# Kernel optimization log

Measured on AMD Instinct MI355X. Metric: run time of the kernel, lower is better.

## Reference

```python
import jax, jax.numpy as jnp
import numpy as np

B, S, D, C = 8, 4096, 512, 2048


def setup_inputs() -> dict:
    key = jax.random.key(0)
    kx, kc = jax.random.split(key)
    x = jax.random.normal(kx, (B, S, D), dtype=jnp.float32)
    # kaiming_uniform_(a=sqrt(5)) on a [*,D,C] tensor ~ U(-bound, bound); exact init
    # distribution is irrelevant for the math, so plain scaled uniform is used.
    bound = 1.0 / np.sqrt(D)
    codebook = jax.random.uniform(kc, (1, 1, D, C), dtype=jnp.float32,
                                  minval=-bound, maxval=bound)
    return {"x": x, "codebook": codebook}


def reference(x, codebook):
    # Original: ((x[..., :, None] - codebook) ** 2).mean(dim=-2) -> [B, S, C]
    # Equivalent GEMM form: mean_d(x_d^2) + mean_d(c_dk^2) - (2/D) * x . c_k
    d = x.shape[-1]
    cb = codebook.reshape(codebook.shape[-2], codebook.shape[-1])  # [D, C]
    x2 = jnp.mean(x * x, axis=-1, keepdims=True)                   # [B, S, 1]
    c2 = jnp.mean(cb * cb, axis=0)                                 # [C]
    xc = jnp.einsum('bsd,dc->bsc', x, cb) / d                      # [B, S, C]
    return x2 + c2 - 2.0 * xc
```

## Files before the change

### kernel.cpp

```cpp
#include <hip/hip_runtime.h>
#include <hip/hip_bf16.h>


typedef __attribute__((ext_vector_type(8))) short bf16x8;
typedef __attribute__((ext_vector_type(4))) float f32x4;

#define M_ROWS 32768
#define K_DIM  512
#define N_COLS 2048

__device__ __forceinline__ unsigned short f2bf(float f) {
    unsigned int u = __float_as_uint(f);
    return (unsigned short)((u + 0x7fffu + ((u >> 16) & 1u)) >> 16);
}

__device__ __forceinline__ void gload_lds16(const void* g, void* l) {
    __builtin_amdgcn_global_load_lds(
        (const __attribute__((address_space(1))) unsigned int*)g,
        (__attribute__((address_space(3))) unsigned int*)l,
        16, 0, 0);
}

__global__ __launch_bounds__(256) void prep_x_kernel(const float* __restrict__ x,
                                                     unsigned short* __restrict__ xb,
                                                     float* __restrict__ x2) {
    const int wid = threadIdx.x >> 6;
    const int lane = threadIdx.x & 63;
    const int row = (blockIdx.x << 2) + wid;
    const float4* p4 = reinterpret_cast<const float4*>(x + (size_t)row * K_DIM);
    float4 v0 = p4[lane];
    float4 v1 = p4[lane + 64];
    float ss = v0.x*v0.x + v0.y*v0.y + v0.z*v0.z + v0.w*v0.w
             + v1.x*v1.x + v1.y*v1.y + v1.z*v1.z + v1.w*v1.w;
    union { unsigned short us[4]; uint2 u2; } pa, pb;
    pa.us[0] = f2bf(v0.x); pa.us[1] = f2bf(v0.y); pa.us[2] = f2bf(v0.z); pa.us[3] = f2bf(v0.w);
    pb.us[0] = f2bf(v1.x); pb.us[1] = f2bf(v1.y); pb.us[2] = f2bf(v1.z); pb.us[3] = f2bf(v1.w);
    uint2* dst = reinterpret_cast<uint2*>(xb + (size_t)row * K_DIM);
    dst[lane]      = pa.u2;
    dst[lane + 64] = pb.u2;
    #pragma unroll
    for (int off = 32; off; off >>= 1) ss += __shfl_xor(ss, off);
    if (lane == 0) x2[row] = ss * (1.0f / (float)K_DIM);
}

__global__ __launch_bounds__(256) void prep_cb_kernel(const float* __restrict__ cb,
                                                      unsigned short* __restrict__ cbT) {
    __shared__ float tile[32][65];
    const int k0 = blockIdx.x * 32;
    const int n0 = blockIdx.y * 64;
    const int tx = threadIdx.x & 63;
    const int ty = threadIdx.x >> 6;
    #pragma unroll
    for (int i = 0; i < 8; ++i) {
        const int k = ty + i * 4;
        tile[k][tx] = cb[(size_t)(k0 + k) * N_COLS + n0 + tx];
    }
    __syncthreads();
    const int kc = threadIdx.x & 31;
    const int nr = threadIdx.x >> 5;
    #pragma unroll
    for (int i = 0; i < 8; ++i) {
        const int n = nr + i * 8;
        cbT[(size_t)(n0 + n) * K_DIM + k0 + kc] = f2bf(tile[kc][n] * 0.00390625f);
    }
}

__global__ __launch_bounds__(256) void c2_kernel(const float* __restrict__ cb,
                                                 float* __restrict__ c2) {
    __shared__ float p[4][64];
    const int t = threadIdx.x;
    const int nl = t & 63;
    const int kc = t >> 6;
    const int n = blockIdx.x * 64 + nl;
    float s = 0.0f;
    for (int k = kc * 128; k < kc * 128 + 128; ++k) {
        float v = cb[(size_t)k * N_COLS + n];
        s += v * v;
    }
    p[kc][nl] = s;
    __syncthreads();
    if (t < 64) {
        c2[blockIdx.x * 64 + t] =
            (p[0][t] + p[1][t] + p[2][t] + p[3][t]) * (1.0f / (float)K_DIM);
    }
}


__device__ __forceinline__ bf16x8 frag_ld(const unsigned short* h, int r, int lhi) {
    const int off = r * 32 + ((lhi ^ ((r >> 1) & 3)) << 3);
    return *reinterpret_cast<const bf16x8*>(&h[off]);
}

#define BAR()  do { asm volatile("" ::: "memory"); \
                    __builtin_amdgcn_s_barrier();  \
                    asm volatile("" ::: "memory"); } while (0)
#define GATE_(n) asm volatile("s_waitcnt vmcnt(" #n ")" ::: "memory")
#define GATE(n) GATE_(n)

__global__ __launch_bounds__(256, 2) void gemm_kernel(
        const unsigned short* __restrict__ A,
        const unsigned short* __restrict__ Bt,
        const float* __restrict__ x2,
        const float* __restrict__ c2,
        float* __restrict__ out) {
    __shared__ unsigned short smem[3][8192];

    const int tid  = threadIdx.x;
    const int wid  = tid >> 6;
    const int lane = tid & 63;
    const int wr64 = (wid >> 1) * 64;
    const int wc64 = (wid & 1) * 64;
    const int l15 = lane & 15;
    const int lhi = lane >> 4;

    const int bid  = blockIdx.x;
    const int lbid = (bid & 7) * 512 + (bid >> 3);
    const int m0 = (lbid >> 4) * 128;
    const int n0 = (lbid & 15) * 128;

    const unsigned short* Ab = A  + (size_t)m0 * K_DIM;
    const unsigned short* Bb = Bt + (size_t)n0 * K_DIM;

    const int c0   = tid;
    const int row0 = c0 >> 2;
    const size_t off0 = (size_t)row0 * K_DIM + ((size_t)(((c0 & 3) ^ ((row0 >> 1) & 3)) * 8));
    const int c1   = 256 + tid;
    const int row1 = c1 >> 2;
    const size_t off1 = (size_t)row1 * K_DIM + ((size_t)(((c1 & 3) ^ ((row1 >> 1) & 3)) * 8));

    f32x4 acc[4][4] = {};

#define STAGE(KT, BUF) do {                                                    \
    gload_lds16(Ab + off0 + (KT) * 32, &smem[(BUF)][wid * 512]);               \
    gload_lds16(Ab + off1 + (KT) * 32, &smem[(BUF)][2048 + wid * 512]);        \
    gload_lds16(Bb + off0 + (KT) * 32, &smem[(BUF)][4096 + wid * 512]);        \
    gload_lds16(Bb + off1 + (KT) * 32, &smem[(BUF)][6144 + wid * 512]); } while (0)

    STAGE(0, 0);
    STAGE(1, 1);
    GATE(4);
    BAR();

    #pragma unroll
    for (int t = 0; t < 16; ++t) {
        if (t < 14) STAGE(t + 2, (t + 2) % 3);
        const unsigned short* cbuf = smem[t % 3];
        bf16x8 b[4];
        #pragma unroll
        for (int nf = 0; nf < 4; ++nf)
            b[nf] = frag_ld(cbuf + 4096, wc64 + nf * 16 + l15, lhi);
        __builtin_amdgcn_s_setprio(1);
        #pragma unroll
        for (int mf = 0; mf < 4; ++mf) {
            const bf16x8 a = frag_ld(cbuf, wr64 + mf * 16 + l15, lhi);
            #pragma unroll
            for (int nf = 0; nf < 4; ++nf)
                acc[mf][nf] = __builtin_amdgcn_mfma_f32_16x16x32_bf16(a, b[nf], acc[mf][nf], 0, 0, 0);
        }
        __builtin_amdgcn_s_setprio(0);
        if (t < 14) { GATE(4); } else if (t == 14) { GATE(0); }
        BAR();
    }
#undef STAGE

    #pragma unroll
    for (int mf = 0; mf < 4; ++mf) {
        const int mrow = m0 + wr64 + mf * 16 + lhi * 4;
        const float xv0 = x2[mrow + 0];
        const float xv1 = x2[mrow + 1];
        const float xv2 = x2[mrow + 2];
        const float xv3 = x2[mrow + 3];
        #pragma unroll
        for (int nf = 0; nf < 4; ++nf) {
            const int col = n0 + wc64 + nf * 16 + l15;
            const float cv = c2[col];
            float* o = out + (size_t)mrow * N_COLS + col;
            o[0 * N_COLS] = xv0 + cv - acc[mf][nf][0];
            o[1 * N_COLS] = xv1 + cv - acc[mf][nf][1];
            o[2 * N_COLS] = xv2 + cv - acc[mf][nf][2];
            o[3 * N_COLS] = xv3 + cv - acc[mf][nf][3];
        }
    }
}

extern "C" void kernel_launch(void* const* d_in, const int* in_sizes, int n_in,
                              void* d_out, int out_size, void* d_ws, size_t ws_size,
                              hipStream_t stream) {
    const float* x  = (const float*)d_in[0];
    const float* cb = (const float*)d_in[1];
    float* out = (float*)d_out;

    char* ws = (char*)d_ws;
    unsigned short* xb  = (unsigned short*)ws;
    unsigned short* cbT = (unsigned short*)(ws + (size_t)33554432);
    float* x2 = (float*)(ws + (size_t)33554432 + 2097152);
    float* c2 = (float*)(ws + (size_t)33554432 + 2097152 + 131072);

    prep_x_kernel<<<M_ROWS / 4, 256, 0, stream>>>(x, xb, x2);
    prep_cb_kernel<<<dim3(16, 32), 256, 0, stream>>>(cb, cbT);
    c2_kernel<<<N_COLS / 64, 256, 0, stream>>>(cb, c2);
    gemm_kernel<<<dim3((M_ROWS / 128) * (N_COLS / 128)), 256, 0, stream>>>(xb, cbT, x2, c2, out);
}
```

Before: 126.9 us.

## Process two N-tiles per block and overlap first tile's stores with second GEMM

Each block now computes two adjacent 128-column output tiles sequentially, running one continuous 32-step K pipeline. The epilogue stores for the first tile are interleaved into the second tile's main loop, so output writes overlap MFMA work instead of sitting in a serial tail. The goal is to hide the large fp32 output write cost. In exchange each block holds two accumulator sets, which raises register pressure and may lower occupancy, and the A tile is reloaded for the second pass.

```diff
diff --git a/kernel.cpp b/kernel.cpp
--- a/kernel.cpp
+++ b/kernel.cpp
@@ -114,12 +114,14 @@
     const int lhi = lane >> 4;
 
     const int bid  = blockIdx.x;
-    const int lbid = (bid & 7) * 512 + (bid >> 3);
-    const int m0 = (lbid >> 4) * 128;
-    const int n0 = (lbid & 15) * 128;
-
-    const unsigned short* Ab = A  + (size_t)m0 * K_DIM;
-    const unsigned short* Bb = Bt + (size_t)n0 * K_DIM;
+    const int lbid = (bid & 7) * 256 + (bid >> 3);
+    const int m0  = (lbid >> 3) * 128;
+    const int n0A = (lbid & 7) * 256;
+    const int n0B = n0A + 128;
+
+    const unsigned short* Ab  = A  + (size_t)m0 * K_DIM;
+    const unsigned short* BbA = Bt + (size_t)n0A * K_DIM;
+    const unsigned short* BbB = Bt + (size_t)n0B * K_DIM;
 
     const int c0   = tid;
     const int row0 = c0 >> 2;
@@ -128,59 +130,91 @@
     const int row1 = c1 >> 2;
     const size_t off1 = (size_t)row1 * K_DIM + ((size_t)(((c1 & 3) ^ ((row1 >> 1) & 3)) * 8));
 
-    f32x4 acc[4][4] = {};
-
-#define STAGE(KT, BUF) do {                                                    \
-    gload_lds16(Ab + off0 + (KT) * 32, &smem[(BUF)][wid * 512]);               \
-    gload_lds16(Ab + off1 + (KT) * 32, &smem[(BUF)][2048 + wid * 512]);        \
-    gload_lds16(Bb + off0 + (KT) * 32, &smem[(BUF)][4096 + wid * 512]);        \
-    gload_lds16(Bb + off1 + (KT) * 32, &smem[(BUF)][6144 + wid * 512]); } while (0)
-
-    STAGE(0, 0);
-    STAGE(1, 1);
+    f32x4 accA[4][4] = {};
+    f32x4 accB[4][4] = {};
+
+    float x2v[16];
+    #pragma unroll
+    for (int mf = 0; mf < 4; ++mf)
+        #pragma unroll
+        for (int jj = 0; jj < 4; ++jj)
+            x2v[mf * 4 + jj] = x2[m0 + wr64 + mf * 16 + lhi * 4 + jj];
+    float c2oA[4];
+    #pragma unroll
+    for (int nf = 0; nf < 4; ++nf) c2oA[nf] = c2[n0A + wc64 + nf * 16 + l15];
+    float* const outA = out + (size_t)(m0 + wr64 + lhi * 4) * N_COLS + n0A + wc64 + l15;
+
+#define STAGE(KT) do {                                                         \
+    const unsigned short* bb_ = ((KT) < 16) ? BbA : BbB;                       \
+    const size_t ko_ = (size_t)(((KT) & 15) * 32);                             \
+    gload_lds16(Ab  + off0 + ko_, &smem[(KT) % 3][wid * 512]);                 \
+    gload_lds16(Ab  + off1 + ko_, &smem[(KT) % 3][2048 + wid * 512]);          \
+    gload_lds16(bb_ + off0 + ko_, &smem[(KT) % 3][4096 + wid * 512]);          \
+    gload_lds16(bb_ + off1 + ko_, &smem[(KT) % 3][6144 + wid * 512]); } while (0)
+
+#define STORE1(IDX) do {                                                       \
+    const int i_ = (IDX);                                                      \
+    const int mf_ = i_ >> 4, nf_ = (i_ >> 2) & 3, jj_ = i_ & 3;                \
+    outA[(size_t)(mf_ * 16 + jj_) * N_COLS + nf_ * 16] =                       \
+        x2v[mf_ * 4 + jj_] + c2oA[nf_] - accA[mf_][nf_][jj_]; } while (0)
+
+#define STEP(S, ACC, GN, DOG, DOST)                                            \
+  {                                                                            \
+    if ((S) <= 29) STAGE((S) + 2);                                             \
+    const unsigned short* cbuf = smem[(S) % 3];                                \
+    bf16x8 b[4];                                                               \
+    _Pragma("unroll")                                                          \
+    for (int nf = 0; nf < 4; ++nf)                                             \
+        b[nf] = frag_ld(cbuf + 4096, wc64 + nf * 16 + l15, lhi);               \
+    __builtin_amdgcn_s_setprio(1);                                             \
+    _Pragma("unroll")                                                          \
+    for (int mf = 0; mf < 4; ++mf) {                                           \
+        const bf16x8 a = frag_ld(cbuf, wr64 + mf * 16 + l15, lhi);             \
+        _Pragma("unroll")                                                      \
+        for (int nf = 0; nf < 4; ++nf)                                         \
+            ACC[mf][nf] = __builtin_amdgcn_mfma_f32_16x16x32_bf16(a, b[nf], ACC[mf][nf], 0, 0, 0); \
+    }                                                                          \
+    __builtin_amdgcn_s_setprio(0);                                             \
+    if (DOG) { GATE(GN); }                                                     \
+    if (DOST) { STORE1(((S) - 16) * 4 + 0); STORE1(((S) - 16) * 4 + 1);        \
+                STORE1(((S) - 16) * 4 + 2); STORE1(((S) - 16) * 4 + 3); }      \
+    BAR();                                                                     \
+  }
+
+    STAGE(0);
+    STAGE(1);
     GATE(4);
     BAR();
 
-    #pragma unroll
-    for (int t = 0; t < 16; ++t) {
-        if (t < 14) STAGE(t + 2, (t + 2) % 3);
-        const unsigned short* cbuf = smem[t % 3];
-        bf16x8 b[4];
+    STEP(0,  accA, 4, 1, 0) STEP(1,  accA, 4, 1, 0) STEP(2,  accA, 4, 1, 0)
+    STEP(3,  accA, 4, 1, 0) STEP(4,  accA, 4, 1, 0) STEP(5,  accA, 4, 1, 0)
+    STEP(6,  accA, 4, 1, 0) STEP(7,  accA, 4, 1, 0) STEP(8,  accA, 4, 1, 0)
+    STEP(9,  accA, 4, 1, 0) STEP(10, accA, 4, 1, 0) STEP(11, accA, 4, 1, 0)
+    STEP(12, accA, 4, 1, 0) STEP(13, accA, 4, 1, 0) STEP(14, accA, 4, 1, 0)
+    STEP(15, accA, 4, 1, 0)
+    STEP(16, accB, 4, 1, 1) STEP(17, accB, 8, 1, 1) STEP(18, accB, 8, 1, 1)
+    STEP(19, accB, 8, 1, 1) STEP(20, accB, 8, 1, 1) STEP(21, accB, 8, 1, 1)
+    STEP(22, accB, 8, 1, 1) STEP(23, accB, 8, 1, 1) STEP(24, accB, 8, 1, 1)
+    STEP(25, accB, 8, 1, 1) STEP(26, accB, 8, 1, 1) STEP(27, accB, 8, 1, 1)
+    STEP(28, accB, 8, 1, 1) STEP(29, accB, 8, 1, 1) STEP(30, accB, 4, 1, 1)
+    STEP(31, accB, 0, 0, 1)
+
+#undef STAGE
+#undef STORE1
+#undef STEP
+
+    float c2oB[4];
+    #pragma unroll
+    for (int nf = 0; nf < 4; ++nf) c2oB[nf] = c2[n0B + wc64 + nf * 16 + l15];
+    float* const outB = out + (size_t)(m0 + wr64 + lhi * 4) * N_COLS + n0B + wc64 + l15;
+    #pragma unroll
+    for (int mf = 0; mf < 4; ++mf)
         #pragma unroll
         for (int nf = 0; nf < 4; ++nf)
-            b[nf] = frag_ld(cbuf + 4096, wc64 + nf * 16 + l15, lhi);
-        __builtin_amdgcn_s_setprio(1);
-        #pragma unroll
-        for (int mf = 0; mf < 4; ++mf) {
-            const bf16x8 a = frag_ld(cbuf, wr64 + mf * 16 + l15, lhi);
             #pragma unroll
-            for (int nf = 0; nf < 4; ++nf)
-                acc[mf][nf] = __builtin_amdgcn_mfma_f32_16x16x32_bf16(a, b[nf], acc[mf][nf], 0, 0, 0);
-        }
-        __builtin_amdgcn_s_setprio(0);
-        if (t < 14) { GATE(4); } else if (t == 14) { GATE(0); }
-        BAR();
-    }
-#undef STAGE
-
-    #pragma unroll
-    for (int mf = 0; mf < 4; ++mf) {
-        const int mrow = m0 + wr64 + mf * 16 + lhi * 4;
-        const float xv0 = x2[mrow + 0];
-        const float xv1 = x2[mrow + 1];
-        const float xv2 = x2[mrow + 2];
-        const float xv3 = x2[mrow + 3];
-        #pragma unroll
-        for (int nf = 0; nf < 4; ++nf) {
-            const int col = n0 + wc64 + nf * 16 + l15;
-            const float cv = c2[col];
-            float* o = out + (size_t)mrow * N_COLS + col;
-            o[0 * N_COLS] = xv0 + cv - acc[mf][nf][0];
-            o[1 * N_COLS] = xv1 + cv - acc[mf][nf][1];
-            o[2 * N_COLS] = xv2 + cv - acc[mf][nf][2];
-            o[3 * N_COLS] = xv3 + cv - acc[mf][nf][3];
-        }
-    }
+            for (int jj = 0; jj < 4; ++jj)
+                outB[(size_t)(mf * 16 + jj) * N_COLS + nf * 16] =
+                    x2v[mf * 4 + jj] + c2oB[nf] - accB[mf][nf][jj];
 }
 
 extern "C" void kernel_launch(void* const* d_in, const int* in_sizes, int n_in,
@@ -199,5 +233,5 @@
     prep_x_kernel<<<M_ROWS / 4, 256, 0, stream>>>(x, xb, x2);
     prep_cb_kernel<<<dim3(16, 32), 256, 0, stream>>>(cb, cbT);
     c2_kernel<<<N_COLS / 64, 256, 0, stream>>>(cb, c2);
-    gemm_kernel<<<dim3((M_ROWS / 128) * (N_COLS / 128)), 256, 0, stream>>>(xb, cbT, x2, c2, out);
-}
+    gemm_kernel<<<dim3((M_ROWS / 128) * (N_COLS / 256)), 256, 0, stream>>>(xb, cbT, x2, c2, out);
+}
```

New measurement: 128.7 us. No clear change (+1.4%).

## Deepen GEMM pipeline to four LDS stages and double-buffer register fragments

Applied to the files above, without the earlier changes.

Grows shared-memory staging from three to four buffers so global-to-LDS loads are issued three K-tiles ahead. The A/B fragments for the next tile are read from LDS into a second register set while MFMAs run on the current set, and the K-loop is manually unrolled with ping-pong register sets. The aim is to hide LDS read latency and global load latency behind matrix math. In exchange it uses more LDS per block and more VGPRs, which may limit occupancy, and the kernel may already be bound by output stores.

```diff
diff --git a/kernel.cpp b/kernel.cpp
--- a/kernel.cpp
+++ b/kernel.cpp
@@ -103,7 +103,7 @@
         const float* __restrict__ x2,
         const float* __restrict__ c2,
         float* __restrict__ out) {
-    __shared__ unsigned short smem[3][8192];
+    __shared__ unsigned short smem[4][8192];
 
     const int tid  = threadIdx.x;
     const int wid  = tid >> 6;
@@ -129,39 +129,60 @@
     const size_t off1 = (size_t)row1 * K_DIM + ((size_t)(((c1 & 3) ^ ((row1 >> 1) & 3)) * 8));
 
     f32x4 acc[4][4] = {};
-
-#define STAGE(KT, BUF) do {                                                    \
-    gload_lds16(Ab + off0 + (KT) * 32, &smem[(BUF)][wid * 512]);               \
-    gload_lds16(Ab + off1 + (KT) * 32, &smem[(BUF)][2048 + wid * 512]);        \
-    gload_lds16(Bb + off0 + (KT) * 32, &smem[(BUF)][4096 + wid * 512]);        \
-    gload_lds16(Bb + off1 + (KT) * 32, &smem[(BUF)][6144 + wid * 512]); } while (0)
-
-    STAGE(0, 0);
-    STAGE(1, 1);
+    bf16x8 aR0[4], bR0[4], aR1[4], bR1[4];
+
+#define STAGE(KT) do {                                                         \
+    gload_lds16(Ab + off0 + (KT) * 32, &smem[(KT) & 3][wid * 512]);            \
+    gload_lds16(Ab + off1 + (KT) * 32, &smem[(KT) & 3][2048 + wid * 512]);     \
+    gload_lds16(Bb + off0 + (KT) * 32, &smem[(KT) & 3][4096 + wid * 512]);     \
+    gload_lds16(Bb + off1 + (KT) * 32, &smem[(KT) & 3][6144 + wid * 512]); } while (0)
+
+#define READF(KT, AR, BR) do {                                                 \
+    const unsigned short* fb_ = smem[(KT) & 3];                                \
+    _Pragma("unroll")                                                          \
+    for (int q = 0; q < 4; ++q) {                                              \
+        AR[q] = frag_ld(fb_,        wr64 + q * 16 + l15, lhi);                 \
+        BR[q] = frag_ld(fb_ + 4096, wc64 + q * 16 + l15, lhi);                 \
+    } } while (0)
+
+#define MFMA16(AR, BR) do {                                                    \
+    __builtin_amdgcn_s_setprio(1);                                             \
+    _Pragma("unroll")                                                          \
+    for (int mf = 0; mf < 4; ++mf)                                             \
+        _Pragma("unroll")                                                      \
+        for (int nf = 0; nf < 4; ++nf)                                         \
+            acc[mf][nf] = __builtin_amdgcn_mfma_f32_16x16x32_bf16(AR[mf], BR[nf], acc[mf][nf], 0, 0, 0); \
+    __builtin_amdgcn_s_setprio(0); } while (0)
+
+#define STEP(T, ARc, BRc, ARn, BRn)                                            \
+  {                                                                            \
+    if ((T) + 3 <= 15) STAGE((T) + 3);                                         \
+    if ((T) < 15) READF((T) + 1, ARn, BRn);                                    \
+    MFMA16(ARc, BRc);                                                          \
+    if ((T) <= 12) { GATE(4); } else if ((T) == 13) { GATE(0); }               \
+    BAR();                                                                     \
+  }
+
+    STAGE(0);
+    STAGE(1);
+    STAGE(2);
     GATE(4);
     BAR();
-
-    #pragma unroll
-    for (int t = 0; t < 16; ++t) {
-        if (t < 14) STAGE(t + 2, (t + 2) % 3);
-        const unsigned short* cbuf = smem[t % 3];
-        bf16x8 b[4];
-        #pragma unroll
-        for (int nf = 0; nf < 4; ++nf)
-            b[nf] = frag_ld(cbuf + 4096, wc64 + nf * 16 + l15, lhi);
-        __builtin_amdgcn_s_setprio(1);
-        #pragma unroll
-        for (int mf = 0; mf < 4; ++mf) {
-            const bf16x8 a = frag_ld(cbuf, wr64 + mf * 16 + l15, lhi);
-            #pragma unroll
-            for (int nf = 0; nf < 4; ++nf)
-                acc[mf][nf] = __builtin_amdgcn_mfma_f32_16x16x32_bf16(a, b[nf], acc[mf][nf], 0, 0, 0);
-        }
-        __builtin_amdgcn_s_setprio(0);
-        if (t < 14) { GATE(4); } else if (t == 14) { GATE(0); }
-        BAR();
-    }
+    READF(0, aR0, bR0);
+
+    STEP(0,  aR0, bR0, aR1, bR1)  STEP(1,  aR1, bR1, aR0, bR0)
+    STEP(2,  aR0, bR0, aR1, bR1)  STEP(3,  aR1, bR1, aR0, bR0)
+    STEP(4,  aR0, bR0, aR1, bR1)  STEP(5,  aR1, bR1, aR0, bR0)
+    STEP(6,  aR0, bR0, aR1, bR1)  STEP(7,  aR1, bR1, aR0, bR0)
+    STEP(8,  aR0, bR0, aR1, bR1)  STEP(9,  aR1, bR1, aR0, bR0)
+    STEP(10, aR0, bR0, aR1, bR1)  STEP(11, aR1, bR1, aR0, bR0)
+    STEP(12, aR0, bR0, aR1, bR1)  STEP(13, aR1, bR1, aR0, bR0)
+    STEP(14, aR0, bR0, aR1, bR1)  STEP(15, aR1, bR1, aR0, bR0)
+
 #undef STAGE
+#undef READF
+#undef MFMA16
+#undef STEP
 
     #pragma unroll
     for (int mf = 0; mf < 4; ++mf) {
```

Result: no change. 127.9 us (+0.7%).
